# Kernel optimization log

Hardware: AMD Instinct MI355X
Metric: run time of the kernel (lower is better)

## Reference

```python
import jax, jax.numpy as jnp
import numpy as np

MIN_NORM = 1e-15
BALL_EPS = 4e-3  # float32 boundary eps used by HGCN PoincareBall


def _norm(x):
    return jnp.clip(jnp.linalg.norm(x, axis=-1, keepdims=True), MIN_NORM, None)


def _artanh(x):
    x = jnp.clip(x, -1.0 + 1e-7, 1.0 - 1e-7)
    return 0.5 * (jnp.log1p(x) - jnp.log1p(-x))


def proj(x, c):
    n = _norm(x)
    maxnorm = (1.0 - BALL_EPS) / jnp.sqrt(c)
    return jnp.where(n > maxnorm, x / n * maxnorm, x)


def expmap0(u, c):
    sc = jnp.sqrt(c)
    n = _norm(u)
    return jnp.tanh(sc * n) * u / (sc * n)


def logmap0(p, c):
    sc = jnp.sqrt(c)
    n = _norm(p)
    return _artanh(sc * n) * p / (sc * n)


def mobius_matvec(W, x, c):
    sc = jnp.sqrt(c)
    xn = _norm(x)
    mx = x @ W.T
    mxn = _norm(mx)
    res = jnp.tanh(mxn / xn * _artanh(sc * xn)) * mx / (mxn * sc)
    cond = jnp.all(mx == 0, axis=-1, keepdims=True)
    return jnp.where(cond, jnp.zeros((), x.dtype), res)


def mobius_add(x, y, c):
    x2 = jnp.sum(x * x, axis=-1, keepdims=True)
    y2 = jnp.sum(y * y, axis=-1, keepdims=True)
    xy = jnp.sum(x * y, axis=-1, keepdims=True)
    num = (1.0 + 2.0 * c * xy + c * y2) * x + (1.0 - c * x2) * y
    den = 1.0 + 2.0 * c * xy + c * c * x2 * y2
    return num / jnp.clip(den, MIN_NORM, None)


N, D_IN, D_OUT, E = 50000, 128, 128, 600000
C_IN, C_OUT = 1.0, 1.0


def setup_inputs() -> dict:
    key = jax.random.key(0)
    k1, k2, k3, k4, k5, k6 = jax.random.split(key, 6)
    x = jax.random.normal(k1, (N, D_IN), dtype=jnp.float32) * 1e-3  # points near ball origin
    x = proj(x, C_IN)
    W = jax.random.normal(k2, (D_OUT, D_IN), dtype=jnp.float32) * (1.0 / np.sqrt(D_IN))
    b = jax.random.normal(k3, (D_OUT,), dtype=jnp.float32) * 1e-3
    edge_w = jax.random.uniform(k4, (E,), dtype=jnp.float32)
    src = jax.random.randint(k5, (E,), 0, N, dtype=jnp.int32)
    dst = jax.random.randint(k6, (E,), 0, N, dtype=jnp.int32)
    return {"x": x, "W": W, "b": b, "edge_w": edge_w, "src": src, "dst": dst}


def reference(x, W, b, edge_w, src, dst):
    # HypLinear (inference: no dropout on weight)
    h = proj(mobius_matvec(W, x, C_IN), C_IN)
    hyp_bias = proj(expmap0(b[None, :], C_IN), C_IN)  # proj_tan0 is identity
    h = proj(mobius_add(h, hyp_bias, C_IN), C_IN)
    # HypAgg (use_att=0): logmap0 -> spmm -> expmap0 -> proj
    xt = logmap0(h, C_IN)                               # [N, D]
    msgs = edge_w[:, None] * xt[src]                    # [E, D] gather
    agg = jax.ops.segment_sum(msgs, dst, num_segments=N)
    h = proj(expmap0(agg, C_IN), C_IN)
    # HypAct: relu in tangent space, re-map with c_out
    t = jax.nn.relu(logmap0(h, C_IN))
    out = proj(expmap0(t, C_OUT), C_OUT)
    return out
```

## Files before the change

### kernel.cpp

```cpp
#include <hip/hip_runtime.h>
#include <math.h>

#define MAXNORM 0.996f
#define MAXDEG 64

typedef _Float16 h2 __attribute__((ext_vector_type(2)));
typedef _Float16 h8v __attribute__((ext_vector_type(8)));
typedef float f4v __attribute__((ext_vector_type(4)));

__device__ __forceinline__ float wave_sum(float v) {
#pragma unroll
  for (int off = 32; off > 0; off >>= 1) v += __shfl_xor(v, off, 64);
  return v;
}

__device__ __forceinline__ float fast_tanh(float x) {
  float e = __expf(2.0f * x);
  return (e - 1.0f) * __builtin_amdgcn_rcpf(e + 1.0f);
}

__device__ __forceinline__ float fast_artanh(float x) {
  x = fminf(x, 1.0f - 1e-7f);
  return 0.5f * __logf((1.0f + x) * __builtin_amdgcn_rcpf(1.0f - x));
}

__device__ __forceinline__ void proj2(float& v0, float& v1) {
  float n = fmaxf(sqrtf(wave_sum(v0 * v0 + v1 * v1)), 1e-15f);
  if (n > MAXNORM) {
    float s = MAXNORM / n;
    v0 *= s;
    v1 *= s;
  }
}

__global__ void k_fill(int* __restrict__ p, int n4) {
  int i = blockIdx.x * blockDim.x + threadIdx.x;
  if (i < n4) ((int4*)p)[i] = make_int4(0, 0, 0, 0);
}

__global__ __launch_bounds__(256, 4) void k_lin_scatter(
    const float* __restrict__ x, const float* __restrict__ W,
    const float* __restrict__ b, const int* __restrict__ src,
    const int* __restrict__ dst, const float* __restrict__ ew,
    int* __restrict__ deg, uint2* __restrict__ csr,
    _Float16* __restrict__ xt, int N, int E, int nbLin) {
  if ((int)blockIdx.x >= nbLin) {
    int id = blockIdx.x - nbLin;
    int stride = (gridDim.x - nbLin) * 256;
    for (int e = id * 256 + threadIdx.x; e < E; e += stride) {
      int d = dst[e];
      int t = atomicAdd(&deg[d], 1);
      csr[((size_t)d << 6) + t] = make_uint2((unsigned)src[e], __float_as_uint(ew[e]));
    }
    return;
  }

  __shared__ _Float16 WsH[128 * 128];
  __shared__ float biasLds[132];
  const int t = threadIdx.x;
  const int lane = t & 63;
  const int wv = t >> 6;

  const float4* W4 = (const float4*)W;
#pragma unroll
  for (int i = 0; i < 16; ++i) {
    int f = t + 256 * i;
    int o = f >> 5;
    int k4 = (f & 31) << 2;
    float4 v = W4[f];
    unsigned lo = __builtin_bit_cast(unsigned, __builtin_amdgcn_cvt_pkrtz(v.x, v.y));
    unsigned hi = __builtin_bit_cast(unsigned, __builtin_amdgcn_cvt_pkrtz(v.z, v.w));
    *(uint2*)&WsH[o * 128 + (k4 ^ ((o & 7) << 3))] = make_uint2(lo, hi);
  }

  if (t < 64) {
    float b0 = b[t], b1 = b[t + 64];
    float nb = fmaxf(sqrtf(wave_sum(b0 * b0 + b1 * b1)), 1e-15f);
    float s = fast_tanh(nb) * __builtin_amdgcn_rcpf(nb);
    float h0 = b0 * s, h1 = b1 * s;
    proj2(h0, h1);
    float y2w = wave_sum(h0 * h0 + h1 * h1);
    biasLds[t] = h0;
    biasLds[t + 64] = h1;
    if (t == 0) biasLds[128] = y2w;
  }
  __syncthreads();

  const int col = lane & 15;
  const int g = lane >> 4;
  float hbv[8];
#pragma unroll
  for (int n = 0; n < 8; ++n) hbv[n] = biasLds[col + 16 * n];
  const float y2 = biasLds[128];

  const int stripe0 = blockIdx.x * 64 + wv * 16;
  int arow = stripe0 + col;
  if (arow >= N) arow = N - 1;
  const float4* X4 = (const float4*)x;

  h8v af[4];
  float pxr = 0.f;
#pragma unroll
  for (int s = 0; s < 4; ++s) {
    float4 a = X4[(size_t)arow * 32 + 8 * s + 2 * g];
    float4 c = X4[(size_t)arow * 32 + 8 * s + 2 * g + 1];
    pxr = fmaf(a.x, a.x, pxr);
    pxr = fmaf(a.y, a.y, pxr);
    pxr = fmaf(a.z, a.z, pxr);
    pxr = fmaf(a.w, a.w, pxr);
    pxr = fmaf(c.x, c.x, pxr);
    pxr = fmaf(c.y, c.y, pxr);
    pxr = fmaf(c.z, c.z, pxr);
    pxr = fmaf(c.w, c.w, pxr);
    union {
      uint4 u;
      h8v h;
    } cv;
    cv.u = make_uint4(
        __builtin_bit_cast(unsigned, __builtin_amdgcn_cvt_pkrtz(a.x, a.y)),
        __builtin_bit_cast(unsigned, __builtin_amdgcn_cvt_pkrtz(a.z, a.w)),
        __builtin_bit_cast(unsigned, __builtin_amdgcn_cvt_pkrtz(c.x, c.y)),
        __builtin_bit_cast(unsigned, __builtin_amdgcn_cvt_pkrtz(c.z, c.w)));
    af[s] = cv.h;
  }
  pxr += __shfl_xor(pxr, 16, 64);
  pxr += __shfl_xor(pxr, 32, 64);

  f4v acc[8];
  const f4v zero = {0.f, 0.f, 0.f, 0.f};
#pragma unroll
  for (int n = 0; n < 8; ++n) acc[n] = zero;

  const int osw = (col & 7) << 3;
#pragma unroll
  for (int n = 0; n < 8; ++n) {
    const int obase = (16 * n + col) * 128;
#pragma unroll
    for (int s = 0; s < 4; ++s) {
      h8v bf = *(const h8v*)&WsH[obase + ((32 * s + 8 * g) ^ osw)];
      acc[n] = __builtin_amdgcn_mfma_f32_16x16x32_f16(af[s], bf, acc[n], 0, 0, 0);
    }
  }

#pragma unroll
  for (int r = 0; r < 4; ++r) {
    float pm = 0.f, pxy = 0.f;
#pragma unroll
    for (int n = 0; n < 8; ++n) {
      float v = acc[n][r];
      pm = fmaf(v, v, pm);
      pxy = fmaf(v, hbv[n], pxy);
    }
#pragma unroll
    for (int off = 1; off < 16; off <<= 1) {
      pm += __shfl_xor(pm, off, 64);
      pxy += __shfl_xor(pxy, off, 64);
    }
    const int irow = g * 4 + r;
    float px = __shfl(pxr, irow, 64);
    float xn = fmaxf(sqrtf(px), 1e-15f);
    float mxn = fmaxf(sqrtf(pm), 1e-15f);
    float s1 = fast_tanh(mxn * __builtin_amdgcn_rcpf(xn) * fast_artanh(xn)) *
               __builtin_amdgcn_rcpf(mxn);
    if (pm == 0.0f) s1 = 0.0f;
    float nv = s1 * mxn;
    if (nv > MAXNORM) {
      s1 *= MAXNORM / nv;
      nv = MAXNORM;
    }
    float x2 = nv * nv;
    float xy = s1 * pxy;
    float A = 1.0f + 2.0f * xy + y2;
    float B = 1.0f - x2;
    float den = fmaxf(1.0f + 2.0f * xy + x2 * y2, 1e-15f);
    float rden = __builtin_amdgcn_rcpf(den);
    float rn2 = fmaxf(A * A * x2 + 2.0f * A * B * xy + B * B * y2, 0.0f);
    float rn = sqrtf(rn2) * rden;
    float gs = 1.0f;
    if (rn > MAXNORM) gs = MAXNORM / rn;
    float ng = fmaxf(fminf(rn, MAXNORM), 1e-15f);
    float slog = fast_artanh(ng) * __builtin_amdgcn_rcpf(ng);
    float ftot = slog * gs * rden;
    float f1 = ftot * A * s1;
    float f2 = ftot * B;
    const int growm = stripe0 + irow;
    if (growm < N) {
      _Float16* dp = xt + (size_t)growm * 128 + col;
#pragma unroll
      for (int n = 0; n < 8; ++n) dp[16 * n] = (_Float16)(f1 * acc[n][r] + f2 * hbv[n]);
    }
  }
}

__global__ __launch_bounds__(256) void k_agg_final(
    const _Float16* __restrict__ xt, const uint2* __restrict__ csr,
    const int* __restrict__ deg, float* __restrict__ out, int N) {
  int n0 = blockIdx.x * 4 + (threadIdx.x >> 6);
  const int lane = threadIdx.x & 63;
  if (n0 >= N) return;
  const int n = __builtin_amdgcn_readfirstlane(n0);
  const int dg = deg[n];
  const uint2* row = csr + ((size_t)n << 6);
  int e = 0;
  float a0 = 0.f, a1 = 0.f;
  for (; e + 8 <= dg; e += 8) {
    uint2 c[8];
#pragma unroll
    for (int i = 0; i < 8; ++i) c[i] = row[e + i];
    h2 u[8];
#pragma unroll
    for (int i = 0; i < 8; ++i) {
      const h2* r = (const h2*)xt + (((size_t)c[i].x) << 6);
      u[i] = r[lane];
    }
#pragma unroll
    for (int i = 0; i < 8; ++i) {
      float w = __uint_as_float(c[i].y);
      a0 = fmaf(w, (float)u[i][0], a0);
      a1 = fmaf(w, (float)u[i][1], a1);
    }
  }
  for (; e < dg; ++e) {
    uint2 c0 = row[e];
    const h2* r = (const h2*)xt + (((size_t)c0.x) << 6);
    h2 u0 = r[lane];
    float w0 = __uint_as_float(c0.y);
    a0 = fmaf(w0, (float)u0[0], a0);
    a1 = fmaf(w0, (float)u0[1], a1);
  }

  float p0 = fmaxf(a0, 0.0f), p1 = fmaxf(a1, 0.0f);
  float an2 = a0 * a0 + a1 * a1;
  float pos2 = p0 * p0 + p1 * p1;
#pragma unroll
  for (int off = 32; off > 0; off >>= 1) {
    an2 += __shfl_xor(an2, off, 64);
    pos2 += __shfl_xor(pos2, off, 64);
  }
  float an = fmaxf(sqrtf(an2), 1e-15f);
  float th = fast_tanh(an);
  float fh = th * __builtin_amdgcn_rcpf(an);
  float hn = th;
  if (th > MAXNORM) {
    fh = MAXNORM * __builtin_amdgcn_rcpf(an);
    hn = MAXNORM;
  }
  float hn_c = fmaxf(hn, 1e-15f);
  float c1 = fh * fast_artanh(hn_c) * __builtin_amdgcn_rcpf(hn_c);
  float tn = fmaxf(c1 * sqrtf(pos2), 1e-15f);
  float ts = fast_tanh(tn);
  float s2 = ts * __builtin_amdgcn_rcpf(tn);
  float gs = 1.0f;
  if (ts > MAXNORM) gs = MAXNORM * __builtin_amdgcn_rcpf(ts);
  float f = s2 * gs * c1;
  ((float2*)(out + (size_t)n * 128))[lane] = make_float2(f * p0, f * p1);
}

__global__ void k_edge(const h2* __restrict__ xt, const float* __restrict__ ew,
                       const int* __restrict__ src, const int* __restrict__ dst,
                       float* __restrict__ agg, int E) {
  int tid = blockIdx.x * blockDim.x + threadIdx.x;
  int gw = tid >> 6;
  int lane = tid & 63;
  int nw = (gridDim.x * blockDim.x) >> 6;
  for (int e = gw; e < E; e += nw) {
    int s = src[e];
    int d = dst[e];
    float wgt = ew[e];
    h2 v = xt[(size_t)s * 64 + lane];
    float* base = agg + (size_t)d * 128 + 2 * lane;
    unsafeAtomicAdd(base, (float)v[0] * wgt);
    unsafeAtomicAdd(base + 1, (float)v[1] * wgt);
  }
}

__global__ void k_final(const float* __restrict__ agg, float* __restrict__ out, int N) {
  int gw = blockIdx.x * 4 + (threadIdx.x >> 6);
  int lane = threadIdx.x & 63;
  if (gw >= N) return;
  float2 v = ((const float2*)(agg + (size_t)gw * 128))[lane];
  float a0 = v.x, a1 = v.y;
  float p0 = fmaxf(a0, 0.0f), p1 = fmaxf(a1, 0.0f);
  float an2 = a0 * a0 + a1 * a1;
  float pos2 = p0 * p0 + p1 * p1;
#pragma unroll
  for (int off = 32; off > 0; off >>= 1) {
    an2 += __shfl_xor(an2, off, 64);
    pos2 += __shfl_xor(pos2, off, 64);
  }
  float an = fmaxf(sqrtf(an2), 1e-15f);
  float th = fast_tanh(an);
  float fh = th * __builtin_amdgcn_rcpf(an);
  float hn = th;
  if (th > MAXNORM) {
    fh = MAXNORM * __builtin_amdgcn_rcpf(an);
    hn = MAXNORM;
  }
  float hn_c = fmaxf(hn, 1e-15f);
  float c1 = fh * fast_artanh(hn_c) * __builtin_amdgcn_rcpf(hn_c);
  float tn = fmaxf(c1 * sqrtf(pos2), 1e-15f);
  float ts = fast_tanh(tn);
  float s2 = ts * __builtin_amdgcn_rcpf(tn);
  float gs = 1.0f;
  if (ts > MAXNORM) gs = MAXNORM * __builtin_amdgcn_rcpf(ts);
  float f = s2 * gs * c1;
  ((float2*)(out + (size_t)gw * 128))[lane] = make_float2(f * p0, f * p1);
}

static inline size_t pad256(size_t x) { return (x + 255) & ~(size_t)255; }

extern "C" void kernel_launch(void* const* d_in, const int* in_sizes, int n_in,
                              void* d_out, int out_size, void* d_ws, size_t ws_size,
                              hipStream_t stream) {
  const float* x = (const float*)d_in[0];
  const float* W = (const float*)d_in[1];
  const float* b = (const float*)d_in[2];
  const float* ew = (const float*)d_in[3];
  const int* src = (const int*)d_in[4];
  const int* dst = (const int*)d_in[5];
  float* out = (float*)d_out;
  const int N = in_sizes[0] / 128;
  const int E = in_sizes[3];

  char* p = (char*)d_ws;
  int* deg = (int*)p;           p += pad256((size_t)N * 4);
  uint2* csr = (uint2*)p;       p += pad256((size_t)N * MAXDEG * 8);
  _Float16* xt = (_Float16*)p;  p += (size_t)N * 256;
  size_t need = (size_t)(p - (char*)d_ws);

  const int nbLin = (N + 63) / 64;
  if (ws_size >= need) {
    const int n4 = (N + 3) / 4;
    k_fill<<<(n4 + 255) / 256, 256, 0, stream>>>(deg, n4);
    k_lin_scatter<<<nbLin + 512, 256, 0, stream>>>(x, W, b, src, dst, ew, deg, csr,
                                                   xt, N, E, nbLin);
    k_agg_final<<<(N + 3) / 4, 256, 0, stream>>>(xt, csr, deg, out, N);
  } else {
    float* agg = (float*)d_ws;
    _Float16* xth = (_Float16*)d_out;
    (void)hipMemsetAsync(agg, 0, (size_t)N * 128 * sizeof(float), stream);
    k_lin_scatter<<<nbLin, 256, 0, stream>>>(x, W, b, nullptr, nullptr, nullptr,
                                             nullptr, nullptr, xth, N, 0, nbLin);
    k_edge<<<2048, 256, 0, stream>>>((const h2*)xth, ew, src, dst, agg, E);
    k_final<<<(N + 3) / 4, 256, 0, stream>>>(agg, out, N);
  }
}
```

Baseline: 90.94 us.

## Pack CSR entries into 32 bits and process two row stripes per block

Each CSR entry now holds a 16-bit source index and a 16-bit quantized edge weight, replacing the 8-byte (src, float weight) pair. This halves CSR write and read traffic in the scatter and aggregation kernels. The linear-layer blocks now each cover two 64-row stripes, which amortizes the shared-memory load of W and the bias setup. The scatter block count is also rebalanced. The change trades weight precision (16-bit quantization) for bandwidth, requires N <= 65536, and adds a guard against degree overflow past MAXDEG.

```diff
diff --git a/kernel.cpp b/kernel.cpp
--- a/kernel.cpp
+++ b/kernel.cpp
@@ -42,7 +42,7 @@
     const float* __restrict__ x, const float* __restrict__ W,
     const float* __restrict__ b, const int* __restrict__ src,
     const int* __restrict__ dst, const float* __restrict__ ew,
-    int* __restrict__ deg, uint2* __restrict__ csr,
+    int* __restrict__ deg, unsigned* __restrict__ csr,
     _Float16* __restrict__ xt, int N, int E, int nbLin) {
   if ((int)blockIdx.x >= nbLin) {
     int id = blockIdx.x - nbLin;
@@ -50,7 +50,10 @@
     for (int e = id * 256 + threadIdx.x; e < E; e += stride) {
       int d = dst[e];
       int t = atomicAdd(&deg[d], 1);
-      csr[((size_t)d << 6) + t] = make_uint2((unsigned)src[e], __float_as_uint(ew[e]));
+      if (t < MAXDEG) {
+        unsigned wq = (unsigned)fmaf(ew[e], 65535.0f, 0.5f);
+        csr[((size_t)d << 6) + t] = (unsigned)src[e] | (wq << 16);
+      }
     }
     return;
   }
@@ -92,139 +95,143 @@
 #pragma unroll
   for (int n = 0; n < 8; ++n) hbv[n] = biasLds[col + 16 * n];
   const float y2 = biasLds[128];
-
-  const int stripe0 = blockIdx.x * 64 + wv * 16;
-  int arow = stripe0 + col;
-  if (arow >= N) arow = N - 1;
   const float4* X4 = (const float4*)x;
-
-  h8v af[4];
-  float pxr = 0.f;
-#pragma unroll
-  for (int s = 0; s < 4; ++s) {
-    float4 a = X4[(size_t)arow * 32 + 8 * s + 2 * g];
-    float4 c = X4[(size_t)arow * 32 + 8 * s + 2 * g + 1];
-    pxr = fmaf(a.x, a.x, pxr);
-    pxr = fmaf(a.y, a.y, pxr);
-    pxr = fmaf(a.z, a.z, pxr);
-    pxr = fmaf(a.w, a.w, pxr);
-    pxr = fmaf(c.x, c.x, pxr);
-    pxr = fmaf(c.y, c.y, pxr);
-    pxr = fmaf(c.z, c.z, pxr);
-    pxr = fmaf(c.w, c.w, pxr);
-    union {
-      uint4 u;
-      h8v h;
-    } cv;
-    cv.u = make_uint4(
-        __builtin_bit_cast(unsigned, __builtin_amdgcn_cvt_pkrtz(a.x, a.y)),
-        __builtin_bit_cast(unsigned, __builtin_amdgcn_cvt_pkrtz(a.z, a.w)),
-        __builtin_bit_cast(unsigned, __builtin_amdgcn_cvt_pkrtz(c.x, c.y)),
-        __builtin_bit_cast(unsigned, __builtin_amdgcn_cvt_pkrtz(c.z, c.w)));
-    af[s] = cv.h;
-  }
-  pxr += __shfl_xor(pxr, 16, 64);
-  pxr += __shfl_xor(pxr, 32, 64);
-
-  f4v acc[8];
-  const f4v zero = {0.f, 0.f, 0.f, 0.f};
-#pragma unroll
-  for (int n = 0; n < 8; ++n) acc[n] = zero;
-
   const int osw = (col & 7) << 3;
-#pragma unroll
-  for (int n = 0; n < 8; ++n) {
-    const int obase = (16 * n + col) * 128;
+
+  for (int half = 0; half < 2; ++half) {
+    const int stripe0 = blockIdx.x * 128 + half * 64 + wv * 16;
+    int arow = stripe0 + col;
+    if (arow >= N) arow = N - 1;
+
+    h8v af[4];
+    float pxr = 0.f;
 #pragma unroll
     for (int s = 0; s < 4; ++s) {
-      h8v bf = *(const h8v*)&WsH[obase + ((32 * s + 8 * g) ^ osw)];
-      acc[n] = __builtin_amdgcn_mfma_f32_16x16x32_f16(af[s], bf, acc[n], 0, 0, 0);
-    }
-  }
-
-#pragma unroll
-  for (int r = 0; r < 4; ++r) {
-    float pm = 0.f, pxy = 0.f;
+      float4 a = X4[(size_t)arow * 32 + 8 * s + 2 * g];
+      float4 c = X4[(size_t)arow * 32 + 8 * s + 2 * g + 1];
+      pxr = fmaf(a.x, a.x, pxr);
+      pxr = fmaf(a.y, a.y, pxr);
+      pxr = fmaf(a.z, a.z, pxr);
+      pxr = fmaf(a.w, a.w, pxr);
+      pxr = fmaf(c.x, c.x, pxr);
+      pxr = fmaf(c.y, c.y, pxr);
+      pxr = fmaf(c.z, c.z, pxr);
+      pxr = fmaf(c.w, c.w, pxr);
+      union {
+        uint4 u;
+        h8v h;
+      } cv;
+      cv.u = make_uint4(
+          __builtin_bit_cast(unsigned, __builtin_amdgcn_cvt_pkrtz(a.x, a.y)),
+          __builtin_bit_cast(unsigned, __builtin_amdgcn_cvt_pkrtz(a.z, a.w)),
+          __builtin_bit_cast(unsigned, __builtin_amdgcn_cvt_pkrtz(c.x, c.y)),
+          __builtin_bit_cast(unsigned, __builtin_amdgcn_cvt_pkrtz(c.z, c.w)));
+      af[s] = cv.h;
+    }
+    pxr += __shfl_xor(pxr, 16, 64);
+    pxr += __shfl_xor(pxr, 32, 64);
+
+    f4v acc[8];
+    const f4v zero = {0.f, 0.f, 0.f, 0.f};
+#pragma unroll
+    for (int n = 0; n < 8; ++n) acc[n] = zero;
+
 #pragma unroll
     for (int n = 0; n < 8; ++n) {
-      float v = acc[n][r];
-      pm = fmaf(v, v, pm);
-      pxy = fmaf(v, hbv[n], pxy);
-    }
-#pragma unroll
-    for (int off = 1; off < 16; off <<= 1) {
-      pm += __shfl_xor(pm, off, 64);
-      pxy += __shfl_xor(pxy, off, 64);
-    }
-    const int irow = g * 4 + r;
-    float px = __shfl(pxr, irow, 64);
-    float xn = fmaxf(sqrtf(px), 1e-15f);
-    float mxn = fmaxf(sqrtf(pm), 1e-15f);
-    float s1 = fast_tanh(mxn * __builtin_amdgcn_rcpf(xn) * fast_artanh(xn)) *
-               __builtin_amdgcn_rcpf(mxn);
-    if (pm == 0.0f) s1 = 0.0f;
-    float nv = s1 * mxn;
-    if (nv > MAXNORM) {
-      s1 *= MAXNORM / nv;
-      nv = MAXNORM;
-    }
-    float x2 = nv * nv;
-    float xy = s1 * pxy;
-    float A = 1.0f + 2.0f * xy + y2;
-    float B = 1.0f - x2;
-    float den = fmaxf(1.0f + 2.0f * xy + x2 * y2, 1e-15f);
-    float rden = __builtin_amdgcn_rcpf(den);
-    float rn2 = fmaxf(A * A * x2 + 2.0f * A * B * xy + B * B * y2, 0.0f);
-    float rn = sqrtf(rn2) * rden;
-    float gs = 1.0f;
-    if (rn > MAXNORM) gs = MAXNORM / rn;
-    float ng = fmaxf(fminf(rn, MAXNORM), 1e-15f);
-    float slog = fast_artanh(ng) * __builtin_amdgcn_rcpf(ng);
-    float ftot = slog * gs * rden;
-    float f1 = ftot * A * s1;
-    float f2 = ftot * B;
-    const int growm = stripe0 + irow;
-    if (growm < N) {
-      _Float16* dp = xt + (size_t)growm * 128 + col;
-#pragma unroll
-      for (int n = 0; n < 8; ++n) dp[16 * n] = (_Float16)(f1 * acc[n][r] + f2 * hbv[n]);
+      const int obase = (16 * n + col) * 128;
+#pragma unroll
+      for (int s = 0; s < 4; ++s) {
+        h8v bf = *(const h8v*)&WsH[obase + ((32 * s + 8 * g) ^ osw)];
+        acc[n] = __builtin_amdgcn_mfma_f32_16x16x32_f16(af[s], bf, acc[n], 0, 0, 0);
+      }
+    }
+
+#pragma unroll
+    for (int r = 0; r < 4; ++r) {
+      float pm = 0.f, pxy = 0.f;
+#pragma unroll
+      for (int n = 0; n < 8; ++n) {
+        float v = acc[n][r];
+        pm = fmaf(v, v, pm);
+        pxy = fmaf(v, hbv[n], pxy);
+      }
+#pragma unroll
+      for (int off = 1; off < 16; off <<= 1) {
+        pm += __shfl_xor(pm, off, 64);
+        pxy += __shfl_xor(pxy, off, 64);
+      }
+      const int irow = g * 4 + r;
+      float px = __shfl(pxr, irow, 64);
+      float xn = fmaxf(sqrtf(px), 1e-15f);
+      float mxn = fmaxf(sqrtf(pm), 1e-15f);
+      float s1 = fast_tanh(mxn * __builtin_amdgcn_rcpf(xn) * fast_artanh(xn)) *
+                 __builtin_amdgcn_rcpf(mxn);
+      if (pm == 0.0f) s1 = 0.0f;
+      float nv = s1 * mxn;
+      if (nv > MAXNORM) {
+        s1 *= MAXNORM / nv;
+        nv = MAXNORM;
+      }
+      float x2 = nv * nv;
+      float xy = s1 * pxy;
+      float A = 1.0f + 2.0f * xy + y2;
+      float B = 1.0f - x2;
+      float den = fmaxf(1.0f + 2.0f * xy + x2 * y2, 1e-15f);
+      float rden = __builtin_amdgcn_rcpf(den);
+      float rn2 = fmaxf(A * A * x2 + 2.0f * A * B * xy + B * B * y2, 0.0f);
+      float rn = sqrtf(rn2) * rden;
+      float gs = 1.0f;
+      if (rn > MAXNORM) gs = MAXNORM / rn;
+      float ng = fmaxf(fminf(rn, MAXNORM), 1e-15f);
+      float slog = fast_artanh(ng) * __builtin_amdgcn_rcpf(ng);
+      float ftot = slog * gs * rden;
+      float f1 = ftot * A * s1;
+      float f2 = ftot * B;
+      const int growm = stripe0 + irow;
+      if (growm < N) {
+        _Float16* dp = xt + (size_t)growm * 128 + col;
+#pragma unroll
+        for (int n = 0; n < 8; ++n) dp[16 * n] = (_Float16)(f1 * acc[n][r] + f2 * hbv[n]);
+      }
     }
   }
 }
 
 __global__ __launch_bounds__(256) void k_agg_final(
-    const _Float16* __restrict__ xt, const uint2* __restrict__ csr,
+    const _Float16* __restrict__ xt, const unsigned* __restrict__ csr,
     const int* __restrict__ deg, float* __restrict__ out, int N) {
   int n0 = blockIdx.x * 4 + (threadIdx.x >> 6);
   const int lane = threadIdx.x & 63;
   if (n0 >= N) return;
   const int n = __builtin_amdgcn_readfirstlane(n0);
-  const int dg = deg[n];
-  const uint2* row = csr + ((size_t)n << 6);
+  int dg = deg[n];
+  if (dg > MAXDEG) dg = MAXDEG;
+  const unsigned* row = csr + ((size_t)n << 6);
   int e = 0;
   float a0 = 0.f, a1 = 0.f;
+  const float wsc = 1.0f / 65535.0f;
   for (; e + 8 <= dg; e += 8) {
-    uint2 c[8];
+    unsigned c[8];
 #pragma unroll
     for (int i = 0; i < 8; ++i) c[i] = row[e + i];
     h2 u[8];
 #pragma unroll
     for (int i = 0; i < 8; ++i) {
-      const h2* r = (const h2*)xt + (((size_t)c[i].x) << 6);
+      const h2* r = (const h2*)xt + (((size_t)(c[i] & 0xFFFFu)) << 6);
       u[i] = r[lane];
     }
 #pragma unroll
     for (int i = 0; i < 8; ++i) {
-      float w = __uint_as_float(c[i].y);
+      float w = (float)(c[i] >> 16) * wsc;
       a0 = fmaf(w, (float)u[i][0], a0);
       a1 = fmaf(w, (float)u[i][1], a1);
     }
   }
   for (; e < dg; ++e) {
-    uint2 c0 = row[e];
-    const h2* r = (const h2*)xt + (((size_t)c0.x) << 6);
+    unsigned c0 = row[e];
+    const h2* r = (const h2*)xt + (((size_t)(c0 & 0xFFFFu)) << 6);
     h2 u0 = r[lane];
-    float w0 = __uint_as_float(c0.y);
+    float w0 = (float)(c0 >> 16) * wsc;
     a0 = fmaf(w0, (float)u0[0], a0);
     a1 = fmaf(w0, (float)u0[1], a1);
   }
@@ -324,16 +331,18 @@
 
   char* p = (char*)d_ws;
   int* deg = (int*)p;           p += pad256((size_t)N * 4);
-  uint2* csr = (uint2*)p;       p += pad256((size_t)N * MAXDEG * 8);
+  unsigned* csr = (unsigned*)p; p += pad256((size_t)N * MAXDEG * 4);
   _Float16* xt = (_Float16*)p;  p += (size_t)N * 256;
   size_t need = (size_t)(p - (char*)d_ws);
 
-  const int nbLin = (N + 63) / 64;
-  if (ws_size >= need) {
+  const int nbLin = (N + 127) / 128;
+  if (ws_size >= need && N <= 65536) {
     const int n4 = (N + 3) / 4;
     k_fill<<<(n4 + 255) / 256, 256, 0, stream>>>(deg, n4);
-    k_lin_scatter<<<nbLin + 512, 256, 0, stream>>>(x, W, b, src, dst, ew, deg, csr,
-                                                   xt, N, E, nbLin);
+    int nbScat = 1024 - (nbLin % 1024);
+    if (nbScat < 256) nbScat += 1024;
+    k_lin_scatter<<<nbLin + nbScat, 256, 0, stream>>>(x, W, b, src, dst, ew, deg, csr,
+                                                      xt, N, E, nbLin);
     k_agg_final<<<(N + 3) / 4, 256, 0, stream>>>(xt, csr, deg, out, N);
   } else {
     float* agg = (float*)d_ws;
```

After: 90.37 us. About the same (-0.6%).
